# Kernel optimization log

Measured on AMD Instinct MI355X. Metric: run time of the kernel, lower is better.

The kernel has to match this reference:

```python
import jax, jax.numpy as jnp
import numpy as np

B, S, D, H = 4, 1024, 1024, 16
DH = D // H
NEG = -10000.0  # mask fill value for non-float32 (bool) masks in the torch code


def setup_inputs() -> dict:
    key = jax.random.key(0)
    ks = jax.random.split(key, 16)
    scale = 0.02
    inp = {
        "query": jax.random.normal(ks[0], (B, S, D), jnp.float32),
        "key": jax.random.normal(ks[1], (B, S, D), jnp.float32),
        "value": jax.random.normal(ks[2], (B, S, D), jnp.float32),
        "pos_embedding": jax.random.normal(ks[3], (B, S, D), jnp.float32),
        # learned params (torch Linear convention: y = x @ W.T + b, W is (out,in))
        "Wq": jax.random.normal(ks[4], (D, D), jnp.float32) * scale,
        "bq": jnp.zeros((D,), jnp.float32),
        "Wk": jax.random.normal(ks[5], (D, D), jnp.float32) * scale,
        "bk": jnp.zeros((D,), jnp.float32),
        "Wv": jax.random.normal(ks[6], (D, D), jnp.float32) * scale,
        "bv": jnp.zeros((D,), jnp.float32),
        "Wpos": jax.random.normal(ks[7], (D, D), jnp.float32) * scale,
        "u_bias": jax.random.normal(ks[8], (H, DH), jnp.float32) * scale,
        "v_bias": jax.random.normal(ks[9], (H, DH), jnp.float32) * scale,
        "Wout": jax.random.normal(ks[10], (D, D), jnp.float32) * scale,
        "bout": jnp.zeros((D,), jnp.float32),
    }
    # right-padding mask: lengths in [S//2, S]; mask[b,i,j] = pad(i) | pad(j)
    lengths = jax.random.randint(ks[11], (B,), S // 2, S + 1)
    pad = jnp.arange(S)[None, :] >= lengths[:, None]  # (B,S)
    inp["mask"] = pad[:, :, None] | pad[:, None, :]  # (B,S,S) bool
    return inp


def _relative_shift(pos_score, mask):
    """Batch-safe Transformer-XL relative shift (vectorized version of the
    per-batch python loop). pos_score: (B,H,S,S), mask: (B,S,S) bool."""
    b, h, s, _ = pos_score.shape
    # per-row true length: S - number of padded rows (column 0 is never padded)
    L = s - jnp.sum(mask[:, :, 0].astype(jnp.int32), axis=-1)  # (B,)
    i = jnp.arange(s)[:, None]
    j = jnp.arange(s)[None, :]

    def shift_one(ps, Lb):  # ps: (H,S,S), Lb: scalar int
        # padded[h,r,0]=0; padded[h,r,k]=ps[h,r,k-1]; flat index of out[i,j] in
        # the (Lb+1, Lb) reshape of padded[:, :Lb, :Lb+1], rows 1: -> offset Lb
        m = Lb + i * Lb + j            # (S,S)
        row = m // (Lb + 1)
        col = m % (Lb + 1)
        g = ps[:, jnp.clip(row, 0, s - 1), jnp.clip(col - 1, 0, s - 1)]  # (H,S,S)
        valid = (i < Lb) & (j < Lb) & (col != 0)
        return jnp.where(valid[None], g, jnp.zeros((), ps.dtype))

    shifted = jax.vmap(shift_one)(pos_score, L)
    # masked_fill_(padding_mask, 0.0)
    return jnp.where(mask[:, None, :, :], jnp.zeros((), pos_score.dtype), shifted)


def reference(query, key, value, pos_embedding, mask,
              Wq, bq, Wk, bk, Wv, bv, Wpos, u_bias, v_bias, Wout, bout):
    b = query.shape[0]
    sqrt_dim = np.sqrt(D).astype(np.float32)

    q = (query @ Wq.T + bq).reshape(b, -1, H, DH)                 # (B,S,H,dh)
    k = (key @ Wk.T + bk).reshape(b, -1, H, DH)                   # (B,S,H,dh)
    v = (value @ Wv.T + bv).reshape(b, -1, H, DH)                 # (B,S,H,dh)
    p = (pos_embedding @ Wpos.T).reshape(b, -1, H, DH)            # (B,S,H,dh)

    content_score = jnp.einsum('bqhd,bkhd->bhqk', q + u_bias, k)  # (B,H,S,S)
    pos_score = jnp.einsum('bqhd,bkhd->bhqk', q + v_bias, p)      # (B,H,S,S)
    pos_score = _relative_shift(pos_score, mask)

    score = (content_score + pos_score) / sqrt_dim
    m4 = mask[:, None, :, :]
    score = jnp.where(m4, NEG, score)
    attn = jax.nn.softmax(score, axis=-1)
    attn = jnp.where(m4, jnp.zeros((), attn.dtype), attn)
    # dropout is identity in eval mode
    context = jnp.einsum('bhqk,bkhd->bqhd', attn, v).reshape(b, -1, D)
    return context @ Wout.T + bout
```

## Files before the change

kernel.cpp:

```cpp
#include <hip/hip_runtime.h>

#define B_ 4
#define S_ 1024
#define D_ 1024
#define H_ 16
#define DH_ 64
#define OOS 0.03125f

#define QPL (1088 * 64)
#define KPL (1024 * 64)
#define VPL (1024 * 64)
#define PPL (200 * 1024)
#define PADLO 1056

#define APL_SW (256 * 32 * 512)
#define WPL_SW (64 * 32 * 512)

typedef __attribute__((ext_vector_type(8))) short short8;
typedef __attribute__((ext_vector_type(4))) float f32x4;
typedef const __attribute__((address_space(1))) unsigned int* gas_t;
typedef __attribute__((address_space(3))) unsigned int* las_t;

__device__ __forceinline__ ushort f2bf(float x) {
  unsigned u = __float_as_uint(x);
  unsigned r = u + 0x7fffu + ((u >> 16) & 1u);
  return (ushort)(r >> 16);
}
__device__ __forceinline__ float bf2f(ushort u) {
  return __uint_as_float(((unsigned)u) << 16);
}

union pack8 { ushort u[8]; uint4 v; };

struct ConvDesc { const float* src; ushort* hi; ushort* lo; };
struct ConvArgs { ConvDesc d[5]; };

__global__ __launch_bounds__(256) void conv_split(ConvArgs args)
{
  const ConvDesc dd = args.d[blockIdx.y];
  const int tt = blockIdx.x;
  const int tid = threadIdx.x;
  const float* src = dd.src + (size_t)tt * 16 * 1024;
  ushort* hi = dd.hi + (size_t)tt * 32 * 512;
  ushort* lo = dd.lo + (size_t)tt * 32 * 512;
#pragma unroll 4
  for (int q = 0; q < 16; ++q) {
    const int s = q * 256 + tid;
    const int r = s >> 8, c4 = s & 255;
    const float4 x = *(const float4*)(src + r * 1024 + c4 * 4);
    const int k = c4 * 4;
    const size_t addr = (size_t)(k >> 5) * 512 + ((k & 31) >> 3) * 128 + r * 8 + (k & 7);
    ushort4 hu, lu;
    hu.x = f2bf(x.x); lu.x = f2bf(x.x - bf2f(hu.x));
    hu.y = f2bf(x.y); lu.y = f2bf(x.y - bf2f(hu.y));
    hu.z = f2bf(x.z); lu.z = f2bf(x.z - bf2f(hu.z));
    hu.w = f2bf(x.w); lu.w = f2bf(x.w - bf2f(hu.w));
    *(ushort4*)(hi + addr) = hu;
    *(ushort4*)(lo + addr) = lu;
  }
}

template <int MODE>
__global__ __launch_bounds__(256, 2) void gemm_bf16x3(
    const ushort* __restrict__ Ahi, const ushort* __restrict__ Alo,
    const ushort* __restrict__ Bhi, const ushort* __restrict__ Blo,
    const float* __restrict__ bias, float* __restrict__ C,
    ushort* __restrict__ O1, ushort* __restrict__ O2,
    const float* __restrict__ ub, const float* __restrict__ vb)
{
  __shared__ __align__(16) ushort SM[12288];
  const int tid = threadIdx.x;
  const int wave = tid >> 6, lane = tid & 63;
  const int m16 = lane & 15, quad = lane >> 4;
  const int mw2 = wave & 1, nw2 = wave >> 1;
  const int mt0 = blockIdx.y * 4;
  const int nt0 = blockIdx.x * 8;

  f32x4 acc[2][4];
#pragma unroll
  for (int mf = 0; mf < 2; ++mf)
#pragma unroll
    for (int nf = 0; nf < 4; ++nf) acc[mf][nf] = (f32x4){0.f, 0.f, 0.f, 0.f};

  for (int kb = 0; kb < 32; ++kb) {
    __syncthreads();
    for (int t = wave; t < 24; t += 4) {
      const ushort* g;
      int l;
      if (t < 4)       { g = Ahi + ((size_t)(mt0 + t) * 32 + kb) * 512;      l = t * 512; }
      else if (t < 8)  { g = Alo + ((size_t)(mt0 + t - 4) * 32 + kb) * 512;  l = 2048 + (t - 4) * 512; }
      else if (t < 16) { g = Bhi + ((size_t)(nt0 + t - 8) * 32 + kb) * 512;  l = 4096 + (t - 8) * 512; }
      else             { g = Blo + ((size_t)(nt0 + t - 16) * 32 + kb) * 512; l = 8192 + (t - 16) * 512; }
      __builtin_amdgcn_global_load_lds((gas_t)(g + lane * 8), (las_t)(SM + l), 16, 0, 0);
    }
    __syncthreads();
    short8 ah[2], al[2], bh[4], bl[4];
#pragma unroll
    for (int mf = 0; mf < 2; ++mf) {
      ah[mf] = *(const short8*)(SM + (mw2 * 2 + mf) * 512 + lane * 8);
      al[mf] = *(const short8*)(SM + 2048 + (mw2 * 2 + mf) * 512 + lane * 8);
    }
#pragma unroll
    for (int nf = 0; nf < 4; ++nf) {
      bh[nf] = *(const short8*)(SM + 4096 + (nw2 * 4 + nf) * 512 + lane * 8);
      bl[nf] = *(const short8*)(SM + 8192 + (nw2 * 4 + nf) * 512 + lane * 8);
    }
#pragma unroll
    for (int mf = 0; mf < 2; ++mf)
#pragma unroll
      for (int nf = 0; nf < 4; ++nf) {
        acc[mf][nf] = __builtin_amdgcn_mfma_f32_16x16x32_bf16(ah[mf], bh[nf], acc[mf][nf], 0, 0, 0);
        acc[mf][nf] = __builtin_amdgcn_mfma_f32_16x16x32_bf16(ah[mf], bl[nf], acc[mf][nf], 0, 0, 0);
        acc[mf][nf] = __builtin_amdgcn_mfma_f32_16x16x32_bf16(al[mf], bh[nf], acc[mf][nf], 0, 0, 0);
      }
  }

  const int Mb = blockIdx.y * 64, Nb = blockIdx.x * 128;
  float* const E = (float*)SM;
#pragma unroll
  for (int c = 0; c < 2; ++c) {
    __syncthreads();
    if (nw2 == c) {
#pragma unroll
      for (int mf = 0; mf < 2; ++mf)
#pragma unroll
        for (int nf = 0; nf < 4; ++nf)
#pragma unroll
          for (int reg = 0; reg < 4; ++reg)
            E[(mw2 * 32 + mf * 16 + quad * 4 + reg) * 64 + nf * 16 + m16] = acc[mf][nf][reg];
    }
    __syncthreads();

    if (MODE == 3) {
#pragma unroll
      for (int q = 0; q < 2; ++q) {
        const int s = tid + 256 * q;
        const int cc = s & 63, rg = s >> 6;
        const int tok0 = Mb + rg * 8;
        const int n = Nb + c * 64 + cc;
        const int bb = tok0 >> 10, jr = tok0 & 1023;
        const int jt = jr >> 6, ksj = (jr >> 5) & 1, qk = (jr >> 3) & 3;
        const int h = n >> 6, dd = n & 63;
        const int subd = dd >> 4, nn = dd & 15;
        const size_t base = (size_t)(bb * 16 + h) * VPL + (size_t)jt * 4096 +
                            (size_t)(subd * 2 + ksj) * 512 + (qk * 16 + nn) * 8;
        const float bvv = bias[n];
        pack8 p;
#pragma unroll
        for (int i = 0; i < 8; ++i) p.u[i] = f2bf(E[(rg * 8 + i) * 64 + cc] + bvv);
        *(uint4*)(O1 + base) = p.v;
      }
    } else {
#pragma unroll
      for (int q = 0; q < 2; ++q) {
        const int s = tid + 256 * q;
        const int r = s >> 3, g = s & 7;
        const int token = Mb + r;
        const int n = Nb + c * 64 + g * 8;
        float v[8];
        *(float4*)&v[0] = *(const float4*)&E[r * 64 + g * 8];
        *(float4*)&v[4] = *(const float4*)&E[r * 64 + g * 8 + 4];
        if (MODE == 0) {
          float4 o0, o1;
          o0.x = v[0] + bias[n + 0]; o0.y = v[1] + bias[n + 1];
          o0.z = v[2] + bias[n + 2]; o0.w = v[3] + bias[n + 3];
          o1.x = v[4] + bias[n + 4]; o1.y = v[5] + bias[n + 5];
          o1.z = v[6] + bias[n + 6]; o1.w = v[7] + bias[n + 7];
          *(float4*)(C + (size_t)token * 1024 + n) = o0;
          *(float4*)(C + (size_t)token * 1024 + n + 4) = o1;
        } else if (MODE == 1) {
          const int bb = token >> 10, sr = token & 1023;
          const int h = n >> 6, d = n & 63;
          const size_t base = (size_t)(bb * 16 + h) * QPL + (size_t)sr * 64 + d;
          pack8 pu, pv;
#pragma unroll
          for (int j = 0; j < 8; ++j) {
            const float qv_ = v[j] + bias[n + j];
            pu.u[j] = f2bf(qv_ + ub[n + j]);
            pv.u[j] = f2bf(qv_ + vb[n + j]);
          }
          *(uint4*)(O1 + base) = pu.v;
          *(uint4*)(O2 + base) = pv.v;
        } else {
          const int bb = token >> 10, jr = token & 1023;
          const int h = n >> 6, dd = n & 63;
          const int ks = dd >> 5, qk = (dd >> 3) & 3;
          size_t base;
          if (MODE == 2)
            base = (size_t)(bb * 16 + h) * KPL + (size_t)(jr >> 6) * 4096 +
                   (size_t)((((jr >> 4) & 3) * 2 + ks)) * 512 + (qk * 16 + (jr & 15)) * 8;
          else {
            const int ro = jr + PADLO;
            base = (size_t)(bb * 16 + h) * PPL + (size_t)(ro >> 4) * 1024 +
                   (size_t)ks * 512 + (qk * 16 + (ro & 15)) * 8;
          }
          pack8 p;
#pragma unroll
          for (int j = 0; j < 8; ++j)
            p.u[j] = f2bf(v[j] + (MODE == 2 ? bias[n + j] : 0.f));
          *(uint4*)(O1 + base) = p.v;
        }
      }
    }
  }
}

__global__ void len_kernel(const int* __restrict__ mask, int* __restrict__ len,
                           ushort* __restrict__ Psw)
{
  const int b = blockIdx.x;
  int cnt = 0;
  for (int i = threadIdx.x; i < S_; i += 256)
    cnt += (mask[(size_t)b * S_ * S_ + (size_t)i * S_] != 0) ? 1 : 0;
  __shared__ int sh[256];
  sh[threadIdx.x] = cnt;
  __syncthreads();
  for (int off = 128; off > 0; off >>= 1) {
    if (threadIdx.x < off) sh[threadIdx.x] += sh[threadIdx.x + off];
    __syncthreads();
  }
  if (threadIdx.x == 0) len[b] = S_ - sh[0];
  for (int idx = threadIdx.x; idx < 16 * 64; idx += 256) {
    const int h = idx >> 6, d = idx & 63;
    Psw[(size_t)(b * 16 + h) * PPL + 65 * 1024 + (d >> 5) * 512 +
        (((d >> 3) & 3) * 16 + 15) * 8 + (d & 7)] = 0;
  }
}

__global__ __launch_bounds__(256, 3) void attn_mfma2(
    const ushort* __restrict__ Qu, const ushort* __restrict__ Qv,
    const ushort* __restrict__ Ksw, const ushort* __restrict__ Vsw,
    const ushort* __restrict__ Psw, const int* __restrict__ len,
    float* __restrict__ CTX)
{
  __shared__ __align__(16) ushort SMEM[22528];
  __shared__ float mrow[32], lrow[32], arow[32];

  ushort* const Ks_  = SMEM;
  ushort* const Vts_ = SMEM + 4096;
  ushort* const P1s_ = SMEM + 8192;
  ushort* const P2s_ = SMEM + 15360;
  float*  const sc   = (float*)(SMEM + 8192);
  ushort* const Pb   = SMEM + 8192 + 4352;

  const int tid  = threadIdx.x;
  const int wave = tid >> 6, lane = tid & 63;
  const int m16  = lane & 15, quad = lane >> 4;
  const int mw   = wave & 1,  nw   = wave >> 1;
  const int koff0 = quad * 8;

  const int i0 = blockIdx.x * 32;
  const int h  = blockIdx.y;
  const int b  = blockIdx.z;
  const int ph = b * 16 + h;
  const int L  = len[b];
  const size_t gb = ((size_t)b * S_) * D_ + h * DH_;

  if (i0 >= L) {
    for (int idx = tid; idx < 32 * 64; idx += 256) {
      const int r = idx >> 6, d = idx & 63;
      CTX[gb + (size_t)(i0 + r) * D_ + d] = 0.f;
    }
    return;
  }

  const ushort* quP = Qu + (size_t)ph * QPL;
  const ushort* qvP = Qv + (size_t)ph * QPL;
  short8 qufr[2][2], qvfr[2][2][2];
#pragma unroll
  for (int Mt = 0; Mt < 2; ++Mt)
#pragma unroll
    for (int ks = 0; ks < 2; ++ks) {
      qufr[Mt][ks] = *(const short8*)(quP + (size_t)(i0 + 16 * Mt + m16) * 64 + ks * 32 + koff0);
#pragma unroll
      for (int off = 0; off < 2; ++off)
        qvfr[off][Mt][ks] =
            *(const short8*)(qvP + (size_t)(i0 + off + 16 * Mt + m16) * 64 + ks * 32 + koff0);
    }

  if (tid < 32) { mrow[tid] = -3.0e38f; lrow[tid] = 0.f; arow[tid] = 0.f; }

  f32x4 ctx0 = {0.f, 0.f, 0.f, 0.f}, ctx1 = {0.f, 0.f, 0.f, 0.f};

  const ushort* ksP = Ksw + (size_t)ph * KPL;
  const ushort* vsP = Vsw + (size_t)ph * VPL;
  const ushort* psP = Psw + (size_t)ph * PPL;

  for (int j0 = 0; j0 < L; j0 += 64) {
    __syncthreads();

    const int jt = j0 >> 6;
    const int A1 = L - 32 - i0 + j0, A2 = j0 - i0 - 33;
    const int ro1 = A1 + PADLO, ro2 = A2 + PADLO;
    const int rb1 = ro1 >> 4, rb2 = ro2 >> 4;
    const int d1 = ro1 & 15, d2 = ro2 & 15;

    {
      const ushort* kgo = ksP + (size_t)jt * 4096;
      const ushort* vgo = vsP + (size_t)jt * 4096;
      const ushort* p1o = psP + (size_t)rb1 * 1024;
      const ushort* p2o = psP + (size_t)rb2 * 1024;
      for (int t = wave; t < 44; t += 4) {
        const ushort* g;
        int l;
        if (t < 8)       { g = kgo + t * 512;        l = t * 512; }
        else if (t < 16) { g = vgo + (t - 8) * 512;  l = 4096 + (t - 8) * 512; }
        else if (t < 30) { g = p1o + (t - 16) * 512; l = 8192 + (t - 16) * 512; }
        else             { g = p2o + (t - 30) * 512; l = 15360 + (t - 30) * 512; }
        __builtin_amdgcn_global_load_lds((gas_t)(g + lane * 8), (las_t)(SMEM + l), 16, 0, 0);
      }
    }
    __syncthreads();

    const int jrem = L - j0;
    const int jmax = (jrem < 64) ? jrem : 64;
    const int cthr = 31 + i0 - j0;

    f32x4 av[9];
#pragma unroll
    for (int t = 0; t < 9; ++t) {
      const int id = wave + 4 * t;
      f32x4 a = {0.f, 0.f, 0.f, 0.f};
      if (id < 8) {
        const int Mt = id & 1, Nt = id >> 1;
        if (16 * Nt < jmax) {
          const ushort* bp = Ks_ + (Nt * 2) * 512 + lane * 8;
          a = __builtin_amdgcn_mfma_f32_16x16x32_bf16(qufr[Mt][0], *(const short8*)bp, a, 0, 0, 0);
          a = __builtin_amdgcn_mfma_f32_16x16x32_bf16(qufr[Mt][1], *(const short8*)(bp + 512), a, 0, 0, 0);
        }
      } else if (id < 22) {
        const int e = id - 8, Mt = e & 1, Ntp = e >> 1;
        const int sm = 16 * (Ntp + Mt);
        if (sm >= d1 + 1 && sm <= jmax + d1 + 30 && 16 * Ntp - d1 <= cthr) {
          const ushort* bp = P1s_ + (Ntp * 2) * 512 + lane * 8;
          a = __builtin_amdgcn_mfma_f32_16x16x32_bf16(qvfr[0][Mt][0], *(const short8*)bp, a, 0, 0, 0);
          a = __builtin_amdgcn_mfma_f32_16x16x32_bf16(qvfr[0][Mt][1], *(const short8*)(bp + 512), a, 0, 0, 0);
        }
      } else {
        const int e = id - 22, Mt = e & 1, Ntp = e >> 1;
        const int sm = 16 * (Ntp + Mt);
        if (sm >= d2 + 1 && sm <= jmax + d2 + 30 && 16 * Ntp + 15 - d2 > cthr) {
          const ushort* bp = P2s_ + (Ntp * 2) * 512 + lane * 8;
          a = __builtin_amdgcn_mfma_f32_16x16x32_bf16(qvfr[1][Mt][0], *(const short8*)bp, a, 0, 0, 0);
          a = __builtin_amdgcn_mfma_f32_16x16x32_bf16(qvfr[1][Mt][1], *(const short8*)(bp + 512), a, 0, 0, 0);
        }
      }
      av[t] = a;
    }
    __syncthreads();

#pragma unroll
    for (int t = 0; t < 9; ++t) {
      const int id = wave + 4 * t;
      if (id < 8) {
        const int Mt = id & 1, Nt = id >> 1;
        if (16 * Nt < jmax) {
#pragma unroll
          for (int reg = 0; reg < 4; ++reg)
            sc[(16 * Mt + quad * 4 + reg) * 68 + 16 * Nt + m16] = av[t][reg];
        }
      }
    }
    __syncthreads();

#pragma unroll
    for (int t = 0; t < 9; ++t) {
      const int id = wave + 4 * t;
      if (id >= 8) {
        const bool isG2 = id >= 22;
        const int e = id - (isG2 ? 22 : 8), Mt = e & 1, Ntp = e >> 1;
        const int dl = isG2 ? d2 : d1;
        const int sm = 16 * (Ntp + Mt);
        const bool use = sm >= dl + 1 && sm <= jmax + dl + 30 &&
                         (isG2 ? (16 * Ntp + 15 - dl > cthr) : (16 * Ntp - dl <= cthr));
        if (use) {
          const int c = 16 * Ntp + m16 - dl;
          const bool sel = isG2 ? (c > cthr) : (c <= cthr);
          if (sel) {
#pragma unroll
            for (int reg = 0; reg < 4; ++reg) {
              const int il = 16 * Mt + quad * 4 + reg;
              const int jl = c - 31 + il;
              if (jl >= 0 && jl < 64) sc[il * 68 + jl] += av[t][reg];
            }
          }
        }
      }
    }
    __syncthreads();

    {
      const int row = tid >> 3, t8 = tid & 7, jb = t8 * 8;
      const float* sr = sc + row * 68 + jb;
      float mx = -3.0e38f;
#pragma unroll
      for (int q = 0; q < 8; ++q)
        if (jb + q < jmax) mx = fmaxf(mx, sr[q]);
#pragma unroll
      for (int off = 1; off < 8; off <<= 1)
        mx = fmaxf(mx, __shfl_xor(mx, off, 64));
      if (t8 == 0) {
        const float mo = mrow[row];
        const float mn = fmaxf(mo, mx);
        arow[row] = __expf((mo - mn) * OOS);
        mrow[row] = mn;
      }
    }
    __syncthreads();
    {
      const int row = tid >> 3, t8 = tid & 7, jb = t8 * 8;
      const float m = mrow[row];
      const float* sr = sc + row * 68 + jb;
      float e[8], s = 0.f;
#pragma unroll
      for (int q = 0; q < 8; ++q) {
        float v = 0.f;
        if (jb + q < jmax) v = __expf((sr[q] - m) * OOS);
        e[q] = v;
        s += v;
      }
      ushort4 u0, u1;
      u0.x = f2bf(e[0]); u0.y = f2bf(e[1]); u0.z = f2bf(e[2]); u0.w = f2bf(e[3]);
      u1.x = f2bf(e[4]); u1.y = f2bf(e[5]); u1.z = f2bf(e[6]); u1.w = f2bf(e[7]);
      *(ushort4*)&Pb[row * 72 + jb] = u0;
      *(ushort4*)&Pb[row * 72 + jb + 4] = u1;
#pragma unroll
      for (int off = 1; off < 8; off <<= 1) s += __shfl_xor(s, off, 64);
      if (t8 == 0) lrow[row] = lrow[row] * arow[row] + s;
    }
    __syncthreads();

    {
      float al[4];
#pragma unroll
      for (int reg = 0; reg < 4; ++reg) al[reg] = arow[16 * mw + quad * 4 + reg];
#pragma unroll
      for (int reg = 0; reg < 4; ++reg) { ctx0[reg] *= al[reg]; ctx1[reg] *= al[reg]; }
      const ushort* ap = Pb + (16 * mw + m16) * 72;
#pragma unroll
      for (int ksj = 0; ksj < 2; ++ksj) {
        const short8 a = *(const short8*)(ap + ksj * 32 + koff0);
        ctx0 = __builtin_amdgcn_mfma_f32_16x16x32_bf16(
            a, *(const short8*)(Vts_ + ((nw * 2) * 2 + ksj) * 512 + lane * 8), ctx0, 0, 0, 0);
        ctx1 = __builtin_amdgcn_mfma_f32_16x16x32_bf16(
            a, *(const short8*)(Vts_ + ((nw * 2 + 1) * 2 + ksj) * 512 + lane * 8), ctx1, 0, 0, 0);
      }
    }
  }

#pragma unroll
  for (int reg = 0; reg < 4; ++reg) {
    const int il = 16 * mw + quad * 4 + reg;
    const int gi = i0 + il;
    const float inv = (gi < L) ? (1.f / lrow[il]) : 0.f;
    CTX[gb + (size_t)gi * D_ + nw * 32 + m16]      = ctx0[reg] * inv;
    CTX[gb + (size_t)gi * D_ + nw * 32 + 16 + m16] = ctx1[reg] * inv;
  }
}

extern "C" void kernel_launch(void* const* d_in, const int* in_sizes, int n_in,
                              void* d_out, int out_size, void* d_ws, size_t ws_size,
                              hipStream_t stream)
{
  (void)in_sizes; (void)n_in; (void)out_size;
  const float* query = (const float*)d_in[0];
  const float* key   = (const float*)d_in[1];
  const float* value = (const float*)d_in[2];
  const float* pos   = (const float*)d_in[3];
  const float* Wq    = (const float*)d_in[4];
  const float* bq    = (const float*)d_in[5];
  const float* Wk    = (const float*)d_in[6];
  const float* bk    = (const float*)d_in[7];
  const float* Wv    = (const float*)d_in[8];
  const float* bv    = (const float*)d_in[9];
  const float* Wpos  = (const float*)d_in[10];
  const float* ub    = (const float*)d_in[11];
  const float* vb    = (const float*)d_in[12];
  const float* Wout  = (const float*)d_in[13];
  const float* bout  = (const float*)d_in[14];
  const int*   mask  = (const int*)d_in[15];

  char* cur = (char*)d_ws;
  auto take = [&](size_t bytes) {
    char* p = cur;
    cur += (bytes + 255) & ~(size_t)255;
    return p;
  };
  float*  CTX = (float*)take((size_t)4096 * 1024 * 4);
  ushort* Qu  = (ushort*)take((size_t)64 * QPL * 2);
  ushort* Qv  = (ushort*)take((size_t)64 * QPL * 2);
  ushort* Ksw = (ushort*)take((size_t)64 * KPL * 2);
  ushort* Vsw = (ushort*)take((size_t)64 * VPL * 2);
  ushort* Psw = (ushort*)take((size_t)64 * PPL * 2);
  ushort* Ah[4], *Al[4];
  for (int i = 0; i < 4; ++i) {
    Ah[i] = (ushort*)take((size_t)APL_SW * 2);
    Al[i] = (ushort*)take((size_t)APL_SW * 2);
  }
  ushort* Wh[5], *Wl[5];
  for (int i = 0; i < 5; ++i) {
    Wh[i] = (ushort*)take((size_t)WPL_SW * 2);
    Wl[i] = (ushort*)take((size_t)WPL_SW * 2);
  }
  int* len = (int*)take(256);
  ushort* Ch = Ah[0];
  ushort* Cl = Al[0];
  if (ws_size < (size_t)(cur - (char*)d_ws)) return;

  len_kernel<<<dim3(B_), dim3(256), 0, stream>>>(mask, len, Psw);

  {
    ConvArgs a;
    a.d[0] = {query, Ah[0], Al[0]};
    a.d[1] = {key,   Ah[1], Al[1]};
    a.d[2] = {value, Ah[2], Al[2]};
    a.d[3] = {pos,   Ah[3], Al[3]};
    a.d[4] = {query, Ah[0], Al[0]};
    conv_split<<<dim3(256, 4), dim3(256), 0, stream>>>(a);
    ConvArgs w;
    w.d[0] = {Wq,   Wh[0], Wl[0]};
    w.d[1] = {Wk,   Wh[1], Wl[1]};
    w.d[2] = {Wv,   Wh[2], Wl[2]};
    w.d[3] = {Wpos, Wh[3], Wl[3]};
    w.d[4] = {Wout, Wh[4], Wl[4]};
    conv_split<<<dim3(64, 5), dim3(256), 0, stream>>>(w);
  }

  const dim3 gblk(256), ggrid(1024 / 128, 4096 / 64);
  gemm_bf16x3<1><<<ggrid, gblk, 0, stream>>>(Ah[0], Al[0], Wh[0], Wl[0], bq, nullptr,
                                             Qu, Qv, ub, vb);
  gemm_bf16x3<2><<<ggrid, gblk, 0, stream>>>(Ah[1], Al[1], Wh[1], Wl[1], bk, nullptr,
                                             Ksw, nullptr, nullptr, nullptr);
  gemm_bf16x3<3><<<ggrid, gblk, 0, stream>>>(Ah[2], Al[2], Wh[2], Wl[2], bv, nullptr,
                                             Vsw, nullptr, nullptr, nullptr);
  gemm_bf16x3<4><<<ggrid, gblk, 0, stream>>>(Ah[3], Al[3], Wh[3], Wl[3], nullptr, nullptr,
                                             Psw, nullptr, nullptr, nullptr);

  attn_mfma2<<<dim3(S_ / 32, H_, B_), dim3(256), 0, stream>>>(
      Qu, Qv, Ksw, Vsw, Psw, len, CTX);

  {
    ConvArgs c;
    c.d[0] = {CTX, Ch, Cl};
    c.d[1] = c.d[0]; c.d[2] = c.d[0]; c.d[3] = c.d[0]; c.d[4] = c.d[0];
    conv_split<<<dim3(256, 1), dim3(256), 0, stream>>>(c);
  }

  gemm_bf16x3<0><<<ggrid, gblk, 0, stream>>>(Ch, Cl, Wh[4], Wl[4], bout, (float*)d_out,
                                             nullptr, nullptr, nullptr, nullptr);
}
```

Before: 729.9 us.

## Process 64 query rows per attention block to share K/V/P tiles

Doubles the attention block from 256 to 512 threads so that two 32-row query halves share one staged copy of the K, V and position tiles per key step. The position-band loads are widened to cover both halves, and each half reads from an offset inside the shared band. This is meant to cut redundant global-to-LDS traffic for K/V/P and halve the grid. In exchange LDS use per block rises, and the whole block now waits on barriers even when one half is past the sequence length and only idles.

```diff
diff --git a/kernel.cpp b/kernel.cpp
--- a/kernel.cpp
+++ b/kernel.cpp
@@ -227,42 +227,45 @@
   }
 }
 
-__global__ __launch_bounds__(256, 3) void attn_mfma2(
+__global__ __launch_bounds__(512, 4) void attn_mfma2(
     const ushort* __restrict__ Qu, const ushort* __restrict__ Qv,
     const ushort* __restrict__ Ksw, const ushort* __restrict__ Vsw,
     const ushort* __restrict__ Psw, const int* __restrict__ len,
     float* __restrict__ CTX)
 {
-  __shared__ __align__(16) ushort SMEM[22528];
-  __shared__ float mrow[32], lrow[32], arow[32];
+  __shared__ __align__(16) ushort SMEM[26624];
+  __shared__ float mrow[64], lrow[64], arow[64];
 
   ushort* const Ks_  = SMEM;
   ushort* const Vts_ = SMEM + 4096;
   ushort* const P1s_ = SMEM + 8192;
-  ushort* const P2s_ = SMEM + 15360;
+  ushort* const P2s_ = SMEM + 17408;
   float*  const sc   = (float*)(SMEM + 8192);
-  ushort* const Pb   = SMEM + 8192 + 4352;
+  ushort* const Pb   = SMEM + 17408;
 
   const int tid  = threadIdx.x;
   const int wave = tid >> 6, lane = tid & 63;
+  const int hw   = wave >> 2, w4 = wave & 3;
   const int m16  = lane & 15, quad = lane >> 4;
-  const int mw   = wave & 1,  nw   = wave >> 1;
+  const int mw   = w4 & 1,  nw   = w4 >> 1;
   const int koff0 = quad * 8;
 
-  const int i0 = blockIdx.x * 32;
+  const int base = blockIdx.x * 64;
+  const int i0 = base + hw * 32;
   const int h  = blockIdx.y;
   const int b  = blockIdx.z;
   const int ph = b * 16 + h;
   const int L  = len[b];
   const size_t gb = ((size_t)b * S_) * D_ + h * DH_;
 
-  if (i0 >= L) {
-    for (int idx = tid; idx < 32 * 64; idx += 256) {
+  if (base >= L) {
+    for (int idx = tid; idx < 64 * 64; idx += 512) {
       const int r = idx >> 6, d = idx & 63;
-      CTX[gb + (size_t)(i0 + r) * D_ + d] = 0.f;
+      CTX[gb + (size_t)(base + r) * D_ + d] = 0.f;
     }
     return;
   }
+  const bool active = (i0 < L);
 
   const ushort* quP = Qu + (size_t)ph * QPL;
   const ushort* qvP = Qv + (size_t)ph * QPL;
@@ -278,7 +281,7 @@
             *(const short8*)(qvP + (size_t)(i0 + off + 16 * Mt + m16) * 64 + ks * 32 + koff0);
     }
 
-  if (tid < 32) { mrow[tid] = -3.0e38f; lrow[tid] = 0.f; arow[tid] = 0.f; }
+  if (tid < 64) { mrow[tid] = -3.0e38f; lrow[tid] = 0.f; arow[tid] = 0.f; }
 
   f32x4 ctx0 = {0.f, 0.f, 0.f, 0.f}, ctx1 = {0.f, 0.f, 0.f, 0.f};
 
@@ -294,19 +297,23 @@
     const int ro1 = A1 + PADLO, ro2 = A2 + PADLO;
     const int rb1 = ro1 >> 4, rb2 = ro2 >> 4;
     const int d1 = ro1 & 15, d2 = ro2 & 15;
+    const int rb1lo = (L - 64 - base + j0 + PADLO) >> 4;
+    const int rb2lo = (j0 - base - 65 + PADLO) >> 4;
+    const ushort* P1h = P1s_ + ((rb1 - rb1lo) << 10);
+    const ushort* P2h = P2s_ + ((rb2 - rb2lo) << 10);
 
     {
       const ushort* kgo = ksP + (size_t)jt * 4096;
       const ushort* vgo = vsP + (size_t)jt * 4096;
-      const ushort* p1o = psP + (size_t)rb1 * 1024;
-      const ushort* p2o = psP + (size_t)rb2 * 1024;
-      for (int t = wave; t < 44; t += 4) {
+      const ushort* p1o = psP + (size_t)rb1lo * 1024;
+      const ushort* p2o = psP + (size_t)rb2lo * 1024;
+      for (int t = wave; t < 52; t += 8) {
         const ushort* g;
         int l;
         if (t < 8)       { g = kgo + t * 512;        l = t * 512; }
         else if (t < 16) { g = vgo + (t - 8) * 512;  l = 4096 + (t - 8) * 512; }
-        else if (t < 30) { g = p1o + (t - 16) * 512; l = 8192 + (t - 16) * 512; }
-        else             { g = p2o + (t - 30) * 512; l = 15360 + (t - 30) * 512; }
+        else if (t < 34) { g = p1o + (t - 16) * 512; l = 8192 + (t - 16) * 512; }
+        else             { g = p2o + (t - 34) * 512; l = 17408 + (t - 34) * 512; }
         __builtin_amdgcn_global_load_lds((gas_t)(g + lane * 8), (las_t)(SMEM + l), 16, 0, 0);
       }
     }
@@ -319,69 +326,74 @@
     f32x4 av[9];
 #pragma unroll
     for (int t = 0; t < 9; ++t) {
-      const int id = wave + 4 * t;
+      const int id = w4 + 4 * t;
       f32x4 a = {0.f, 0.f, 0.f, 0.f};
+      if (active) {
+        if (id < 8) {
+          const int Mt = id & 1, Nt = id >> 1;
+          if (16 * Nt < jmax) {
+            const ushort* bp = Ks_ + (Nt * 2) * 512 + lane * 8;
+            a = __builtin_amdgcn_mfma_f32_16x16x32_bf16(qufr[Mt][0], *(const short8*)bp, a, 0, 0, 0);
+            a = __builtin_amdgcn_mfma_f32_16x16x32_bf16(qufr[Mt][1], *(const short8*)(bp + 512), a, 0, 0, 0);
+          }
+        } else if (id < 22) {
+          const int e = id - 8, Mt = e & 1, Ntp = e >> 1;
+          const int sm = 16 * (Ntp + Mt);
+          if (sm >= d1 + 1 && sm <= jmax + d1 + 30 && 16 * Ntp - d1 <= cthr) {
+            const ushort* bp = P1h + (Ntp * 2) * 512 + lane * 8;
+            a = __builtin_amdgcn_mfma_f32_16x16x32_bf16(qvfr[0][Mt][0], *(const short8*)bp, a, 0, 0, 0);
+            a = __builtin_amdgcn_mfma_f32_16x16x32_bf16(qvfr[0][Mt][1], *(const short8*)(bp + 512), a, 0, 0, 0);
+          }
+        } else {
+          const int e = id - 22, Mt = e & 1, Ntp = e >> 1;
+          const int sm = 16 * (Ntp + Mt);
+          if (sm >= d2 + 1 && sm <= jmax + d2 + 30 && 16 * Ntp + 15 - d2 > cthr) {
+            const ushort* bp = P2h + (Ntp * 2) * 512 + lane * 8;
+            a = __builtin_amdgcn_mfma_f32_16x16x32_bf16(qvfr[1][Mt][0], *(const short8*)bp, a, 0, 0, 0);
+            a = __builtin_amdgcn_mfma_f32_16x16x32_bf16(qvfr[1][Mt][1], *(const short8*)(bp + 512), a, 0, 0, 0);
+          }
+        }
+      }
+      av[t] = a;
+    }
+    __syncthreads();
+
+#pragma unroll
+    for (int t = 0; t < 2; ++t) {
+      const int id = w4 + 4 * t;
       if (id < 8) {
         const int Mt = id & 1, Nt = id >> 1;
         if (16 * Nt < jmax) {
-          const ushort* bp = Ks_ + (Nt * 2) * 512 + lane * 8;
-          a = __builtin_amdgcn_mfma_f32_16x16x32_bf16(qufr[Mt][0], *(const short8*)bp, a, 0, 0, 0);
-          a = __builtin_amdgcn_mfma_f32_16x16x32_bf16(qufr[Mt][1], *(const short8*)(bp + 512), a, 0, 0, 0);
+#pragma unroll
+          for (int reg = 0; reg < 4; ++reg)
+            sc[(hw * 32 + 16 * Mt + quad * 4 + reg) * 68 + 16 * Nt + m16] =
+                active ? av[t][reg] : 0.f;
         }
-      } else if (id < 22) {
-        const int e = id - 8, Mt = e & 1, Ntp = e >> 1;
-        const int sm = 16 * (Ntp + Mt);
-        if (sm >= d1 + 1 && sm <= jmax + d1 + 30 && 16 * Ntp - d1 <= cthr) {
-          const ushort* bp = P1s_ + (Ntp * 2) * 512 + lane * 8;
-          a = __builtin_amdgcn_mfma_f32_16x16x32_bf16(qvfr[0][Mt][0], *(const short8*)bp, a, 0, 0, 0);
-          a = __builtin_amdgcn_mfma_f32_16x16x32_bf16(qvfr[0][Mt][1], *(const short8*)(bp + 512), a, 0, 0, 0);
-        }
-      } else {
-        const int e = id - 22, Mt = e & 1, Ntp = e >> 1;
-        const int sm = 16 * (Ntp + Mt);
-        if (sm >= d2 + 1 && sm <= jmax + d2 + 30 && 16 * Ntp + 15 - d2 > cthr) {
-          const ushort* bp = P2s_ + (Ntp * 2) * 512 + lane * 8;
-          a = __builtin_amdgcn_mfma_f32_16x16x32_bf16(qvfr[1][Mt][0], *(const short8*)bp, a, 0, 0, 0);
-          a = __builtin_amdgcn_mfma_f32_16x16x32_bf16(qvfr[1][Mt][1], *(const short8*)(bp + 512), a, 0, 0, 0);
-        }
-      }
-      av[t] = a;
-    }
-    __syncthreads();
-
-#pragma unroll
-    for (int t = 0; t < 9; ++t) {
-      const int id = wave + 4 * t;
-      if (id < 8) {
-        const int Mt = id & 1, Nt = id >> 1;
-        if (16 * Nt < jmax) {
-#pragma unroll
-          for (int reg = 0; reg < 4; ++reg)
-            sc[(16 * Mt + quad * 4 + reg) * 68 + 16 * Nt + m16] = av[t][reg];
-        }
-      }
-    }
-    __syncthreads();
-
-#pragma unroll
-    for (int t = 0; t < 9; ++t) {
-      const int id = wave + 4 * t;
-      if (id >= 8) {
-        const bool isG2 = id >= 22;
-        const int e = id - (isG2 ? 22 : 8), Mt = e & 1, Ntp = e >> 1;
-        const int dl = isG2 ? d2 : d1;
-        const int sm = 16 * (Ntp + Mt);
-        const bool use = sm >= dl + 1 && sm <= jmax + dl + 30 &&
-                         (isG2 ? (16 * Ntp + 15 - dl > cthr) : (16 * Ntp - dl <= cthr));
-        if (use) {
-          const int c = 16 * Ntp + m16 - dl;
-          const bool sel = isG2 ? (c > cthr) : (c <= cthr);
-          if (sel) {
-#pragma unroll
-            for (int reg = 0; reg < 4; ++reg) {
-              const int il = 16 * Mt + quad * 4 + reg;
-              const int jl = c - 31 + il;
-              if (jl >= 0 && jl < 64) sc[il * 68 + jl] += av[t][reg];
+      }
+    }
+    __syncthreads();
+
+    if (active) {
+#pragma unroll
+      for (int t = 0; t < 9; ++t) {
+        const int id = w4 + 4 * t;
+        if (id >= 8) {
+          const bool isG2 = id >= 22;
+          const int e = id - (isG2 ? 22 : 8), Mt = e & 1, Ntp = e >> 1;
+          const int dl = isG2 ? d2 : d1;
+          const int sm = 16 * (Ntp + Mt);
+          const bool use = sm >= dl + 1 && sm <= jmax + dl + 30 &&
+                           (isG2 ? (16 * Ntp + 15 - dl > cthr) : (16 * Ntp - dl <= cthr));
+          if (use) {
+            const int c = 16 * Ntp + m16 - dl;
+            const bool sel = isG2 ? (c > cthr) : (c <= cthr);
+            if (sel) {
+#pragma unroll
+              for (int reg = 0; reg < 4; ++reg) {
+                const int il = 16 * Mt + quad * 4 + reg;
+                const int jl = c - 31 + il;
+                if (jl >= 0 && jl < 64) sc[(hw * 32 + il) * 68 + jl] += av[t][reg];
+              }
             }
           }
         }
@@ -430,13 +442,13 @@
     }
     __syncthreads();
 
-    {
+    if (active) {
       float al[4];
 #pragma unroll
-      for (int reg = 0; reg < 4; ++reg) al[reg] = arow[16 * mw + quad * 4 + reg];
+      for (int reg = 0; reg < 4; ++reg) al[reg] = arow[hw * 32 + 16 * mw + quad * 4 + reg];
 #pragma unroll
       for (int reg = 0; reg < 4; ++reg) { ctx0[reg] *= al[reg]; ctx1[reg] *= al[reg]; }
-      const ushort* ap = Pb + (16 * mw + m16) * 72;
+      const ushort* ap = Pb + (hw * 32 + 16 * mw + m16) * 72;
 #pragma unroll
       for (int ksj = 0; ksj < 2; ++ksj) {
         const short8 a = *(const short8*)(ap + ksj * 32 + koff0);
@@ -452,7 +464,7 @@
   for (int reg = 0; reg < 4; ++reg) {
     const int il = 16 * mw + quad * 4 + reg;
     const int gi = i0 + il;
-    const float inv = (gi < L) ? (1.f / lrow[il]) : 0.f;
+    const float inv = (active && gi < L) ? (1.f / lrow[hw * 32 + il]) : 0.f;
     CTX[gb + (size_t)gi * D_ + nw * 32 + m16]      = ctx0[reg] * inv;
     CTX[gb + (size_t)gi * D_ + nw * 32 + 16 + m16] = ctx1[reg] * inv;
   }
@@ -536,7 +548,7 @@
   gemm_bf16x3<4><<<ggrid, gblk, 0, stream>>>(Ah[3], Al[3], Wh[3], Wl[3], nullptr, nullptr,
                                              Psw, nullptr, nullptr, nullptr);
 
-  attn_mfma2<<<dim3(S_ / 32, H_, B_), dim3(256), 0, stream>>>(
+  attn_mfma2<<<dim3(S_ / 64, H_, B_), dim3(512), 0, stream>>>(
       Qu, Qv, Ksw, Vsw, Psw, len, CTX);
 
   {
```

New measurement: 734.3 us. No clear change (+0.6%).
